# Kernel optimization log

Hardware: AMD Instinct MI355X
Metric: run time of the kernel (lower is better)

Reference implementation:

```python
import jax, jax.numpy as jnp
import numpy as np

IN_F = 2048
OUT_F = 2048
BATCH = 8192
ACT_BITS = 4
EPS = 1e-5


def setup_inputs() -> dict:
    key = jax.random.key(0)
    kx, kw, kb = jax.random.split(key, 3)
    x = jax.random.normal(kx, (BATCH, IN_F), dtype=jnp.float32)
    # kaiming-uniform-like init: bound = sqrt(6/fan_in) with a=sqrt(5) -> gain sqrt(2/(1+5))
    bound_w = float(np.sqrt(6.0 / (1.0 + 5.0)) / np.sqrt(IN_F))
    weight = jax.random.uniform(kw, (OUT_F, IN_F), minval=-bound_w, maxval=bound_w, dtype=jnp.float32)
    bound_b = float(1.0 / np.sqrt(IN_F))
    bias = jax.random.uniform(kb, (OUT_F,), minval=-bound_b, maxval=bound_b, dtype=jnp.float32)
    return {"x": x, "weight": weight, "bias": bias}


def _ste_sign(x):
    return x + jax.lax.stop_gradient(jnp.sign(x) - x)


def _ste_clip(x, lo, hi):
    return x + jax.lax.stop_gradient(jnp.clip(x, lo, hi) - x)


def reference(x, weight, bias):
    # weight binarization (ternary-ish via sign of mean-centered rows)
    w_centered = weight - jnp.mean(weight, axis=1, keepdims=True)
    w_bin = _ste_sign(w_centered)                       # [out, in]
    beta = jnp.mean(jnp.abs(weight), axis=1)[None, :]   # [1, out]
    # layer norm (no affine) over last dim
    mu = jnp.mean(x, axis=-1, keepdims=True)
    var = jnp.mean((x - mu) ** 2, axis=-1, keepdims=True)
    xln = (x - mu) / jnp.sqrt(var + EPS)
    qb = float(2 ** (ACT_BITS - 1) - 1)
    gama = jnp.maximum(jnp.max(jnp.abs(xln), axis=-1, keepdims=True), EPS)  # [B,1]
    xq = _ste_clip(xln * (qb / gama), -qb + EPS, qb - EPS)
    y = jnp.einsum('bi,oi->bo', xq, w_bin)
    y = y * (beta * gama / qb)
    return y + bias
```

## Files before the change

kernel.cpp:

```cpp
#include <hip/hip_runtime.h>
#include <hip/hip_bf16.h>

#define BATCH 8192
#define IN_F  2048
#define OUT_F 2048
#define QB    7.0f
#define EPSV  1e-5f
#define ASCALE 18.0f

typedef char  i8x4 __attribute__((ext_vector_type(4)));
typedef int   i32x4 __attribute__((ext_vector_type(4)));

#define AS1(p) ((__attribute__((address_space(1))) void*)(p))
#define AS3(p) ((__attribute__((address_space(3))) void*)(p))

__device__ __forceinline__ float waveReduceSum(float v) {
#pragma unroll
  for (int off = 32; off > 0; off >>= 1) v += __shfl_xor(v, off, 64);
  return v;
}
__device__ __forceinline__ float waveReduceMax(float v) {
#pragma unroll
  for (int off = 32; off > 0; off >>= 1) v = fmaxf(v, __shfl_xor(v, off, 64));
  return v;
}

__global__ __launch_bounds__(256) void prep_kernel(const float* __restrict__ x,
                                                   const float* __restrict__ w,
                                                   char* __restrict__ xq,
                                                   char* __restrict__ wb,
                                                   float* __restrict__ gamaOut,
                                                   float* __restrict__ betaOut) {
  __shared__ float red[8];
  const int t = threadIdx.x;
  const int wave = t >> 6, lane = t & 63;

  if (blockIdx.x < OUT_F) {
    const int row = blockIdx.x;
    const float* wr = w + (size_t)row * IN_F;
    float4 v0 = ((const float4*)wr)[t];
    float4 v1 = ((const float4*)wr)[t + 256];
    float s  = v0.x + v0.y + v0.z + v0.w + v1.x + v1.y + v1.z + v1.w;
    float sa = fabsf(v0.x) + fabsf(v0.y) + fabsf(v0.z) + fabsf(v0.w)
             + fabsf(v1.x) + fabsf(v1.y) + fabsf(v1.z) + fabsf(v1.w);
    float wsum = waveReduceSum(s);
    float wsa  = waveReduceSum(sa);
    if (lane == 0) { red[wave] = wsum; red[4 + wave] = wsa; }
    __syncthreads();
    const float mu   = (red[0] + red[1] + red[2] + red[3]) * (1.0f / IN_F);
    const float beta = (red[4] + red[5] + red[6] + red[7]) * (1.0f / IN_F);
    if (t == 0) betaOut[row] = beta;

    char* wbr = wb + (size_t)row * IN_F;
    auto sgn = [&](float xv) -> char {
      float d = xv - mu;
      return (char)((d > 0.0f) ? 1 : (d < 0.0f ? -1 : 0));
    };
    i8x4 q0 = { sgn(v0.x), sgn(v0.y), sgn(v0.z), sgn(v0.w) };
    i8x4 q1 = { sgn(v1.x), sgn(v1.y), sgn(v1.z), sgn(v1.w) };
    ((i8x4*)wbr)[t]       = q0;
    ((i8x4*)wbr)[t + 256] = q1;
  } else {
    const int row = blockIdx.x - OUT_F;
    const float* xr = x + (size_t)row * IN_F;
    float4 v0 = ((const float4*)xr)[t];
    float4 v1 = ((const float4*)xr)[t + 256];
    float s  = v0.x + v0.y + v0.z + v0.w + v1.x + v1.y + v1.z + v1.w;
    float s2 = v0.x*v0.x + v0.y*v0.y + v0.z*v0.z + v0.w*v0.w
             + v1.x*v1.x + v1.y*v1.y + v1.z*v1.z + v1.w*v1.w;
    float wsum  = waveReduceSum(s);
    float wsum2 = waveReduceSum(s2);
    if (lane == 0) { red[wave] = wsum; red[4 + wave] = wsum2; }
    __syncthreads();
    const float mu  = (red[0] + red[1] + red[2] + red[3]) * (1.0f / IN_F);
    const float ex2 = (red[4] + red[5] + red[6] + red[7]) * (1.0f / IN_F);
    const float rstd = rsqrtf(fmaxf(ex2 - mu * mu, 0.0f) + EPSV);

    float n[8];
    n[0] = (v0.x - mu) * rstd; n[1] = (v0.y - mu) * rstd;
    n[2] = (v0.z - mu) * rstd; n[3] = (v0.w - mu) * rstd;
    n[4] = (v1.x - mu) * rstd; n[5] = (v1.y - mu) * rstd;
    n[6] = (v1.z - mu) * rstd; n[7] = (v1.w - mu) * rstd;
    float amax = 0.0f;
#pragma unroll
    for (int j = 0; j < 8; ++j) amax = fmaxf(amax, fabsf(n[j]));

    __syncthreads();
    float wmax = waveReduceMax(amax);
    if (lane == 0) red[wave] = wmax;
    __syncthreads();
    const float g = fmaxf(fmaxf(fmaxf(red[0], red[1]), fmaxf(red[2], red[3])), EPSV);
    if (t == 0) gamaOut[row] = g;

    const float qs = (QB * ASCALE) / g;
    const float lo = (-QB + EPSV) * ASCALE, hi = (QB - EPSV) * ASCALE;
    auto qz = [&](float v) -> char {
      return (char)__float2int_rn(fminf(fmaxf(v * qs, lo), hi));
    };
    char* xqr = xq + (size_t)row * IN_F;
    i8x4 q0 = { qz(n[0]), qz(n[1]), qz(n[2]), qz(n[3]) };
    i8x4 q1 = { qz(n[4]), qz(n[5]), qz(n[6]), qz(n[7]) };
    ((i8x4*)xqr)[t]       = q0;
    ((i8x4*)xqr)[t + 256] = q1;
  }
}

__global__ __launch_bounds__(256) void gemm_kernel(const char* __restrict__ A,
                                                   const char* __restrict__ B,
                                                   const float* __restrict__ beta,
                                                   const float* __restrict__ gama,
                                                   const float* __restrict__ bias,
                                                   float* __restrict__ out) {
  __shared__ __align__(16) char As[128 * 128];
  __shared__ __align__(16) char Bs[128 * 128];

  const int t = threadIdx.x;
  const int wave = t >> 6, lane = t & 63;
  const int mBase = blockIdx.y * 128;
  const int nBase = blockIdx.x * 128;
  const int wm = (wave >> 1) * 64;
  const int wn = (wave & 1) * 64;

  i32x4 acc[4][4];
#pragma unroll
  for (int i = 0; i < 4; ++i)
#pragma unroll
    for (int j = 0; j < 4; ++j) {
      i32x4 z = {0, 0, 0, 0};
      acc[i][j] = z;
    }

  const int lr = lane >> 3;
  const int ls = lane & 7;
  const int gch = (ls - lr) & 7;
  const char* aG[4];
  const char* bG[4];
  char* aL[4];
  char* bL[4];
#pragma unroll
  for (int j = 0; j < 4; ++j) {
    const int rowInTile = j * 32 + wave * 8 + lr;
    aG[j] = A + (size_t)(mBase + rowInTile) * IN_F + gch * 16;
    bG[j] = B + (size_t)(nBase + rowInTile) * IN_F + gch * 16;
    aL[j] = As + (j * 32 + wave * 8) * 128;
    bL[j] = Bs + (j * 32 + wave * 8) * 128;
  }

  const int fr = lane & 15;
  const int kq = lane >> 4;
  const char* aF = As + (wm + fr) * 128;
  const char* bF = Bs + (wn + fr) * 128;
  int koff[2];
#pragma unroll
  for (int ks = 0; ks < 2; ++ks) koff[ks] = ((ks * 4 + kq + fr) & 7) * 16;

  for (int k0 = 0; k0 < IN_F; k0 += 128) {
#pragma unroll
    for (int j = 0; j < 4; ++j) {
      __builtin_amdgcn_global_load_lds(AS1(aG[j] + k0), AS3(aL[j]), 16, 0, 0);
      __builtin_amdgcn_global_load_lds(AS1(bG[j] + k0), AS3(bL[j]), 16, 0, 0);
    }
    __syncthreads();

#pragma unroll
    for (int ks = 0; ks < 2; ++ks) {
      i32x4 af[4], bf[4];
#pragma unroll
      for (int mi = 0; mi < 4; ++mi) af[mi] = *(const i32x4*)(aF + mi * 16 * 128 + koff[ks]);
#pragma unroll
      for (int ni = 0; ni < 4; ++ni) bf[ni] = *(const i32x4*)(bF + ni * 16 * 128 + koff[ks]);
#pragma unroll
      for (int mi = 0; mi < 4; ++mi)
#pragma unroll
        for (int ni = 0; ni < 4; ++ni)
          acc[mi][ni] = __builtin_amdgcn_mfma_i32_16x16x64_i8(af[mi], bf[ni], acc[mi][ni], 0, 0, 0);
    }
    __syncthreads();
  }

  const float qinv = 1.0f / (QB * ASCALE);
  const int orow0 = mBase + wm + (kq << 2);
  const int ocol0 = nBase + wn + fr;
#pragma unroll
  for (int mi = 0; mi < 4; ++mi) {
    const int rbase = orow0 + mi * 16;
    const float g0 = gama[rbase + 0] * qinv;
    const float g1 = gama[rbase + 1] * qinv;
    const float g2 = gama[rbase + 2] * qinv;
    const float g3 = gama[rbase + 3] * qinv;
#pragma unroll
    for (int ni = 0; ni < 4; ++ni) {
      const int c = ocol0 + ni * 16;
      const float bsc = beta[c];
      const float bv  = bias[c];
      float* op = out + (size_t)rbase * OUT_F + c;
      op[0 * OUT_F] = (float)acc[mi][ni][0] * (bsc * g0) + bv;
      op[1 * OUT_F] = (float)acc[mi][ni][1] * (bsc * g1) + bv;
      op[2 * OUT_F] = (float)acc[mi][ni][2] * (bsc * g2) + bv;
      op[3 * OUT_F] = (float)acc[mi][ni][3] * (bsc * g3) + bv;
    }
  }
}

extern "C" void kernel_launch(void* const* d_in, const int* in_sizes, int n_in,
                              void* d_out, int out_size, void* d_ws, size_t ws_size,
                              hipStream_t stream) {
  const float* x      = (const float*)d_in[0];
  const float* weight = (const float*)d_in[1];
  const float* bias   = (const float*)d_in[2];
  float* out = (float*)d_out;

  char* ws = (char*)d_ws;
  char* wbin = ws;
  char* xq   = ws + (size_t)OUT_F * IN_F;
  float* betaW = (float*)(ws + (size_t)OUT_F * IN_F + (size_t)BATCH * IN_F);
  float* gamaX = betaW + OUT_F;

  prep_kernel<<<OUT_F + BATCH, 256, 0, stream>>>(x, weight, xq, wbin, gamaX, betaW);
  gemm_kernel<<<dim3(OUT_F / 128, BATCH / 128), 256, 0, stream>>>(xq, wbin, betaW, gamaX, bias, out);
}
```

Baseline: 170.7 us.

## Double-buffer LDS with 256x256 tiles, 8 waves, and swizzled block order

```diff
diff --git a/kernel.cpp b/kernel.cpp
--- a/kernel.cpp
+++ b/kernel.cpp
@@ -105,25 +105,27 @@
   }
 }
 
-__global__ __launch_bounds__(256) void gemm_kernel(const char* __restrict__ A,
+__global__ __launch_bounds__(512) void gemm_kernel(const char* __restrict__ A,
                                                    const char* __restrict__ B,
                                                    const float* __restrict__ beta,
                                                    const float* __restrict__ gama,
                                                    const float* __restrict__ bias,
                                                    float* __restrict__ out) {
-  __shared__ __align__(16) char As[128 * 128];
-  __shared__ __align__(16) char Bs[128 * 128];
+  __shared__ __align__(16) char As[2 * 256 * 128];
+  __shared__ __align__(16) char Bs[2 * 256 * 128];
 
   const int t = threadIdx.x;
   const int wave = t >> 6, lane = t & 63;
-  const int mBase = blockIdx.y * 128;
-  const int nBase = blockIdx.x * 128;
-  const int wm = (wave >> 1) * 64;
-  const int wn = (wave & 1) * 64;
-
-  i32x4 acc[4][4];
-#pragma unroll
-  for (int i = 0; i < 4; ++i)
+  const int bid = blockIdx.x;
+  const int swz = (bid & 7) * 32 + (bid >> 3);
+  const int mBase = (swz >> 3) * 256;
+  const int nBase = (swz & 7) * 256;
+  const int wm = (wave >> 2) * 128;
+  const int wn = (wave & 3) * 64;
+
+  i32x4 acc[8][4];
+#pragma unroll
+  for (int i = 0; i < 8; ++i)
 #pragma unroll
     for (int j = 0; j < 4; ++j) {
       i32x4 z = {0, 0, 0, 0};
@@ -135,54 +137,69 @@
   const int gch = (ls - lr) & 7;
   const char* aG[4];
   const char* bG[4];
-  char* aL[4];
-  char* bL[4];
+  int lOff[4];
 #pragma unroll
   for (int j = 0; j < 4; ++j) {
-    const int rowInTile = j * 32 + wave * 8 + lr;
+    const int rowInTile = j * 64 + wave * 8 + lr;
     aG[j] = A + (size_t)(mBase + rowInTile) * IN_F + gch * 16;
     bG[j] = B + (size_t)(nBase + rowInTile) * IN_F + gch * 16;
-    aL[j] = As + (j * 32 + wave * 8) * 128;
-    bL[j] = Bs + (j * 32 + wave * 8) * 128;
+    lOff[j] = (j * 64 + wave * 8) * 128;
   }
 
   const int fr = lane & 15;
   const int kq = lane >> 4;
-  const char* aF = As + (wm + fr) * 128;
-  const char* bF = Bs + (wn + fr) * 128;
   int koff[2];
 #pragma unroll
   for (int ks = 0; ks < 2; ++ks) koff[ks] = ((ks * 4 + kq + fr) & 7) * 16;
 
-  for (int k0 = 0; k0 < IN_F; k0 += 128) {
+  auto stage = [&](int k0, int buf) {
 #pragma unroll
     for (int j = 0; j < 4; ++j) {
-      __builtin_amdgcn_global_load_lds(AS1(aG[j] + k0), AS3(aL[j]), 16, 0, 0);
-      __builtin_amdgcn_global_load_lds(AS1(bG[j] + k0), AS3(bL[j]), 16, 0, 0);
+      __builtin_amdgcn_global_load_lds(AS1(aG[j] + k0), AS3(As + buf * 32768 + lOff[j]), 16, 0, 0);
+      __builtin_amdgcn_global_load_lds(AS1(bG[j] + k0), AS3(Bs + buf * 32768 + lOff[j]), 16, 0, 0);
     }
-    __syncthreads();
-
-#pragma unroll
-    for (int ks = 0; ks < 2; ++ks) {
-      i32x4 af[4], bf[4];
-#pragma unroll
-      for (int mi = 0; mi < 4; ++mi) af[mi] = *(const i32x4*)(aF + mi * 16 * 128 + koff[ks]);
-#pragma unroll
-      for (int ni = 0; ni < 4; ++ni) bf[ni] = *(const i32x4*)(bF + ni * 16 * 128 + koff[ks]);
-#pragma unroll
-      for (int mi = 0; mi < 4; ++mi)
-#pragma unroll
-        for (int ni = 0; ni < 4; ++ni)
-          acc[mi][ni] = __builtin_amdgcn_mfma_i32_16x16x64_i8(af[mi], bf[ni], acc[mi][ni], 0, 0, 0);
-    }
-    __syncthreads();
-  }
+  };
+  auto compute = [&](int buf) {
+    const char* aF = As + buf * 32768 + (wm + fr) * 128;
+    const char* bF = Bs + buf * 32768 + (wn + fr) * 128;
+    i32x4 af0[8], bf0[4], af1[8], bf1[4];
+#pragma unroll
+    for (int ni = 0; ni < 4; ++ni) bf0[ni] = *(const i32x4*)(bF + ni * 2048 + koff[0]);
+#pragma unroll
+    for (int mi = 0; mi < 8; ++mi) af0[mi] = *(const i32x4*)(aF + mi * 2048 + koff[0]);
+#pragma unroll
+    for (int ni = 0; ni < 4; ++ni) bf1[ni] = *(const i32x4*)(bF + ni * 2048 + koff[1]);
+#pragma unroll
+    for (int mi = 0; mi < 8; ++mi) af1[mi] = *(const i32x4*)(aF + mi * 2048 + koff[1]);
+#pragma unroll
+    for (int mi = 0; mi < 8; ++mi)
+#pragma unroll
+      for (int ni = 0; ni < 4; ++ni)
+        acc[mi][ni] = __builtin_amdgcn_mfma_i32_16x16x64_i8(af0[mi], bf0[ni], acc[mi][ni], 0, 0, 0);
+#pragma unroll
+    for (int mi = 0; mi < 8; ++mi)
+#pragma unroll
+      for (int ni = 0; ni < 4; ++ni)
+        acc[mi][ni] = __builtin_amdgcn_mfma_i32_16x16x64_i8(af1[mi], bf1[ni], acc[mi][ni], 0, 0, 0);
+  };
+
+  stage(0, 0);
+  __syncthreads();
+
+  int cur = 0;
+  for (int k0 = 128; k0 < IN_F; k0 += 128) {
+    stage(k0, cur ^ 1);
+    compute(cur);
+    __syncthreads();
+    cur ^= 1;
+  }
+  compute(cur);
 
   const float qinv = 1.0f / (QB * ASCALE);
   const int orow0 = mBase + wm + (kq << 2);
   const int ocol0 = nBase + wn + fr;
 #pragma unroll
-  for (int mi = 0; mi < 4; ++mi) {
+  for (int mi = 0; mi < 8; ++mi) {
     const int rbase = orow0 + mi * 16;
     const float g0 = gama[rbase + 0] * qinv;
     const float g1 = gama[rbase + 1] * qinv;
@@ -217,5 +234,5 @@
   float* gamaX = betaW + OUT_F;
 
   prep_kernel<<<OUT_F + BATCH, 256, 0, stream>>>(x, weight, xq, wbin, gamaX, betaW);
-  gemm_kernel<<<dim3(OUT_F / 128, BATCH / 128), 256, 0, stream>>>(xq, wbin, betaW, gamaX, bias, out);
-}
+  gemm_kernel<<<(OUT_F / 256) * (BATCH / 256), 512, 0, stream>>>(xq, wbin, betaW, gamaX, bias, out);
+}
```

Measured after the change: 158.3 us. 7.2% less time.
